# Kernel optimization log

Measured on AMD Instinct MI355X. Metric: run time of the kernel, lower is better.

## Reference

```python
import jax, jax.numpy as jnp
import numpy as np

EPS = 0.01  # eigenvalue cutoff in vstars_from_quadrics


def _cluster(predicted_points, samples, normals):
    # predicted_points: [B,M,3]; samples, normals: [B,N,3]
    B, N, _ = samples.shape
    M = predicted_points.shape[1]

    # --- knn_points with k=1: argmin_m ||s_n - p_m||^2 = argmin_m (|p_m|^2 - 2 s.p) ---
    dots = jnp.einsum('bnd,bmd->bnm', samples, predicted_points)      # [B,N,M]
    pp2 = jnp.sum(predicted_points * predicted_points, axis=-1)       # [B,M]
    closest_idx = jnp.argmin(pp2[:, None, :] - 2.0 * dots, axis=-1)   # [B,N] int

    # --- per-sample plane quadric (ps ps^T), ps = [n, -n.s] ---
    ds = -jnp.sum(normals * samples, axis=-1)                          # [B,N]
    ps = jnp.concatenate([normals, ds[..., None]], axis=-1)            # [B,N,4]
    quadrics = (ps[..., :, None] * ps[..., None, :]).reshape(B, N, 16)  # [B,N,16]

    # --- scatter_mean into M voronoi bins (zero default for empty bins) ---
    seg_sum = jax.vmap(lambda v, i: jax.ops.segment_sum(v, i, num_segments=M))
    q_sum = seg_sum(quadrics, closest_idx)                              # [B,M,16]
    n_sum = seg_sum(normals, closest_idx)                               # [B,M,3]
    cnt = seg_sum(jnp.ones((B, N, 1), quadrics.dtype), closest_idx)     # [B,M,1]
    denom = jnp.maximum(cnt, 1.0)
    target_quadrics = (q_sum / denom).reshape(B, M, 4, 4)
    mean_normals = n_sum / denom

    non_void = jnp.sum(mean_normals * mean_normals, axis=-1) > 0        # [B,M] bool

    # --- vstars_from_quadrics (computed densely, masked where bin is empty) ---
    A = target_quadrics[..., :3, :3]                                    # [B,M,3,3]
    bvec = -target_quadrics[..., 3, :3]                                 # [B,M,3]
    # void bins -> A == 0; substitute a well-conditioned matrix so SVD is safe,
    # result is masked to 0 anyway (rhs is 0 there as well).
    fake = jnp.diag(jnp.asarray([3.0, 2.0, 1.0], A.dtype))
    A_safe = jnp.where(non_void[..., None, None], A, fake)
    u, eigs, vh = jnp.linalg.svd(A_safe)                                # eigs desc
    ratio = eigs / jnp.maximum(eigs[..., 0:1], 1e-20)
    mask_s = ratio > EPS
    eigs2 = jnp.where(mask_s, 1.0 / jnp.where(mask_s, eigs, 1.0), 0.0)  # [B,M,3]
    rhs = bvec - jnp.einsum('bmij,bmj->bmi', A, predicted_points)       # b - A p
    t = jnp.einsum('bmji,bmj->bmi', u, rhs)                             # U^T rhs
    delta = jnp.einsum('bmji,bmj->bmi', vh, eigs2 * t)                  # Vh^T D U^T rhs
    vstars = predicted_points + delta
    vstars = jnp.where(non_void[..., None], vstars, 0.0)
    return A, mean_normals, vstars, non_void


def setup_inputs() -> dict:
    key = jax.random.key(0)
    k1, k2, k3 = jax.random.split(key, 3)
    B, M, N = 4, 1024, 65536
    predicted_points = jax.random.normal(k1, (B, M, 3), dtype=jnp.float32)
    samples = jax.random.normal(k2, (B, N, 3), dtype=jnp.float32)
    normals = jax.random.normal(k3, (B, N, 3), dtype=jnp.float32)
    normals = normals / jnp.linalg.norm(normals, axis=-1, keepdims=True)
    return {"predicted_points": predicted_points, "samples": samples, "normals": normals}


def reference(predicted_points, samples, normals):
    target_As, mean_normals, vstars, non_void = _cluster(predicted_points, samples, normals)
    return target_As, mean_normals, vstars, non_void
```

## Files before the change

kernel.cpp:

```cpp
#include <hip/hip_runtime.h>
#include <hip/hip_cooperative_groups.h>

namespace cg = cooperative_groups;

#define BB 4
#define MM 1024
#define NN 65536
#define CL (BB * MM)

#define ROTJ(APP, AQQ, APQ, ARP, ARQ, V0P, V1P, V2P, V0Q, V1Q, V2Q)            \
    do {                                                                       \
        double apq_ = APQ;                                                     \
        if (fabs(apq_) > 1e-300) {                                             \
            double theta_ = (AQQ - APP) / (2.0 * apq_);                        \
            double t_ = 1.0 / (fabs(theta_) + sqrt(theta_ * theta_ + 1.0));    \
            if (theta_ < 0.0) t_ = -t_;                                        \
            double c_ = 1.0 / sqrt(t_ * t_ + 1.0), sn_ = t_ * c_;              \
            APP -= t_ * apq_; AQQ += t_ * apq_; APQ = 0.0;                     \
            double arp_ = ARP, arq_ = ARQ;                                     \
            ARP = c_ * arp_ - sn_ * arq_;                                      \
            ARQ = sn_ * arp_ + c_ * arq_;                                      \
            double x_;                                                         \
            x_ = V0P; V0P = c_ * x_ - sn_ * V0Q; V0Q = sn_ * x_ + c_ * V0Q;    \
            x_ = V1P; V1P = c_ * x_ - sn_ * V1Q; V1Q = sn_ * x_ + c_ * V1Q;    \
            x_ = V2P; V2P = c_ * x_ - sn_ * V2Q; V2Q = sn_ * x_ + c_ * V2Q;    \
        }                                                                      \
    } while (0)

#define CESWAP(EI, EJ, VA, VB, VC, WA, WB, WC)                                 \
    do {                                                                       \
        if (EI < EJ) {                                                         \
            double tt_;                                                        \
            tt_ = EI; EI = EJ; EJ = tt_;                                       \
            tt_ = VA; VA = WA; WA = tt_;                                       \
            tt_ = VB; VB = WB; WB = tt_;                                       \
            tt_ = VC; VC = WC; WC = tt_;                                       \
        }                                                                      \
    } while (0)

__device__ __forceinline__ void cluster_body(
    int wave, int lane, const float* __restrict__ pp,
    const float* __restrict__ smp, const float* __restrict__ nrm,
    const int* __restrict__ head, const int* __restrict__ next,
    float* __restrict__ out)
{
    const int bc = wave >> 10;
    const int* NX = next + (size_t)bc * NN;
    const float* Sc = smp + (size_t)bc * NN * 3;
    const float* Nr = nrm + (size_t)bc * NN * 3;

    double q00 = 0, q01 = 0, q02 = 0, q11 = 0, q12 = 0, q22 = 0;
    double nd0 = 0, nd1 = 0, nd2 = 0, s0 = 0, s1 = 0, s2 = 0;
    int count = 0;

    int cur = head[wave * 64 + lane];
    while (cur >= 0) {
        double sxv = Sc[cur * 3 + 0], syv = Sc[cur * 3 + 1], szv = Sc[cur * 3 + 2];
        double nx = Nr[cur * 3 + 0], ny = Nr[cur * 3 + 1], nz = Nr[cur * 3 + 2];
        double d = -(nx * sxv + ny * syv + nz * szv);
        q00 += nx * nx; q01 += nx * ny; q02 += nx * nz;
        q11 += ny * ny; q12 += ny * nz; q22 += nz * nz;
        nd0 += nx * d; nd1 += ny * d; nd2 += nz * d;
        s0 += nx; s1 += ny; s2 += nz;
        ++count;
        cur = NX[cur];
    }
#pragma unroll
    for (int o = 32; o > 0; o >>= 1) {
        q00 += __shfl_xor(q00, o); q01 += __shfl_xor(q01, o); q02 += __shfl_xor(q02, o);
        q11 += __shfl_xor(q11, o); q12 += __shfl_xor(q12, o); q22 += __shfl_xor(q22, o);
        nd0 += __shfl_xor(nd0, o); nd1 += __shfl_xor(nd1, o); nd2 += __shfl_xor(nd2, o);
        s0  += __shfl_xor(s0, o);  s1  += __shfl_xor(s1, o);  s2  += __shfl_xor(s2, o);
        count += __shfl_xor(count, o);
    }

    double denom = count > 1 ? (double)count : 1.0;
    double A00 = q00 / denom, A01 = q01 / denom, A02 = q02 / denom;
    double A11 = q11 / denom, A12 = q12 / denom, A22 = q22 / denom;
    double mn0 = s0 / denom, mn1 = s1 / denom, mn2 = s2 / denom;
    double bv0 = -nd0 / denom, bv1 = -nd1 / denom, bv2 = -nd2 / denom;
    bool nonvoid = (mn0 * mn0 + mn1 * mn1 + mn2 * mn2) > 0.0;

    double vs0 = 0, vs1 = 0, vs2 = 0;
    if (nonvoid) {
        double a00 = A00, a01 = A01, a02 = A02, a11 = A11, a12 = A12, a22 = A22;
        double v00 = 1, v01 = 0, v02 = 0;
        double v10 = 0, v11 = 1, v12 = 0;
        double v20 = 0, v21 = 0, v22 = 1;
#pragma unroll
        for (int sweep = 0; sweep < 8; ++sweep) {
            ROTJ(a00, a11, a01, a02, a12, v00, v10, v20, v01, v11, v21);
            ROTJ(a00, a22, a02, a01, a12, v00, v10, v20, v02, v12, v22);
            ROTJ(a11, a22, a12, a01, a02, v01, v11, v21, v02, v12, v22);
        }
        double e0 = a00, e1 = a11, e2 = a22;
        CESWAP(e0, e1, v00, v10, v20, v01, v11, v21);
        CESWAP(e0, e2, v00, v10, v20, v02, v12, v22);
        CESWAP(e1, e2, v01, v11, v21, v02, v12, v22);

        double emax = e0 > 1e-20 ? e0 : 1e-20;
        const float* Pp = pp + (size_t)wave * 3;
        double px = Pp[0], py = Pp[1], pz = Pp[2];
        double r0 = bv0 - (A00 * px + A01 * py + A02 * pz);
        double r1 = bv1 - (A01 * px + A11 * py + A12 * pz);
        double r2 = bv2 - (A02 * px + A12 * py + A22 * pz);
        double thr = 0.01 * emax;
        if (e0 > thr) { double w = (v00 * r0 + v10 * r1 + v20 * r2) / e0; vs0 += w * v00; vs1 += w * v10; vs2 += w * v20; }
        if (e1 > thr) { double w = (v01 * r0 + v11 * r1 + v21 * r2) / e1; vs0 += w * v01; vs1 += w * v11; vs2 += w * v21; }
        if (e2 > thr) { double w = (v02 * r0 + v12 * r1 + v22 * r2) / e2; vs0 += w * v02; vs1 += w * v12; vs2 += w * v22; }
        vs0 += px; vs1 += py; vs2 += pz;
    }

    if (lane == 0) {
        float* Ao = out + (size_t)wave * 9;
        Ao[0] = (float)A00; Ao[1] = (float)A01; Ao[2] = (float)A02;
        Ao[3] = (float)A01; Ao[4] = (float)A11; Ao[5] = (float)A12;
        Ao[6] = (float)A02; Ao[7] = (float)A12; Ao[8] = (float)A22;
        float* Mo = out + 36864 + (size_t)wave * 3;
        Mo[0] = (float)mn0; Mo[1] = (float)mn1; Mo[2] = (float)mn2;
        float* Vo = out + 49152 + (size_t)wave * 3;
        Vo[0] = (float)vs0; Vo[1] = (float)vs1; Vo[2] = (float)vs2;
        out[61440 + wave] = nonvoid ? 1.0f : 0.0f;
    }
}

__global__ __launch_bounds__(512, 4) void k_fused(
    const float* __restrict__ pp, const float* __restrict__ smp,
    const float* __restrict__ nrm, int* __restrict__ head,
    int* __restrict__ next, float* __restrict__ out)
{
    cg::grid_group grid = cg::this_grid();

    __shared__ float4 pts[MM];
    __shared__ float bestSh[8][256];
    __shared__ int   biSh[8][256];

    head[blockIdx.x * 512 + threadIdx.x] = -1;
    const int b   = blockIdx.x >> 7;
    const int blk = blockIdx.x & 127;
    const float* P = pp + b * MM * 3;
    for (int i = threadIdx.x; i < MM; i += 512) {
        float x = P[i * 3 + 0], y = P[i * 3 + 1], z = P[i * 3 + 2];
        pts[i] = make_float4(x, y, z, x * x + y * y + z * z);
    }
    grid.sync();

    const int l = threadIdx.x & 63;
    const int g = threadIdx.x >> 6;
    const float* S = smp + (size_t)b * NN * 3;

    for (int half = 0; half < 2; ++half) {
        const int nb = blk * 512 + half * 256;
        float ax[4], ay[4], az[4], best[4];
        int bi[4];
#pragma unroll
        for (int j = 0; j < 4; ++j) {
            int n = nb + j * 64 + l;
            ax[j] = -2.0f * S[n * 3 + 0];
            ay[j] = -2.0f * S[n * 3 + 1];
            az[j] = -2.0f * S[n * 3 + 2];
            best[j] = 3.4e38f;
            bi[j] = 0;
        }
        const int m0 = g * 128;
#pragma unroll 4
        for (int mi = 0; mi < 128; ++mi) {
            float4 p = pts[m0 + mi];
#pragma unroll
            for (int j = 0; j < 4; ++j) {
                float sc = fmaf(ax[j], p.x, fmaf(ay[j], p.y, fmaf(az[j], p.z, p.w)));
                if (sc < best[j]) { best[j] = sc; bi[j] = m0 + mi; }
            }
        }
#pragma unroll
        for (int j = 0; j < 4; ++j) {
            bestSh[g][j * 64 + l] = best[j];
            biSh[g][j * 64 + l]   = bi[j];
        }
        __syncthreads();

        if (threadIdx.x < 256) {
            const int t = threadIdx.x;
            float bb = bestSh[0][t];
            int   ii = biSh[0][t];
#pragma unroll
            for (int gg = 1; gg < 8; ++gg) {
                float bo = bestSh[gg][t];
                int   io = biSh[gg][t];
                if (bo < bb) { bb = bo; ii = io; }
            }
            const int n = nb + t;
            const int gc = b * MM + ii;
            next[(size_t)b * NN + n] = atomicExch(&head[gc * 64 + (t & 63)], n);
        }
        __syncthreads();
    }
    __threadfence();
    grid.sync();

    cluster_body(blockIdx.x * 8 + g, l, pp, smp, nrm, head, next, out);
}

__global__ __launch_bounds__(256) void k_clear(int4* __restrict__ head4)
{
    head4[blockIdx.x * 256 + threadIdx.x] = make_int4(-1, -1, -1, -1);
}

__global__ __launch_bounds__(512) void k_assign(
    const float* __restrict__ pp, const float* __restrict__ smp,
    int* __restrict__ head, int* __restrict__ next)
{
    __shared__ float4 pts[MM];
    __shared__ float bestSh[8][256];
    __shared__ int   biSh[8][256];

    const int b   = blockIdx.x >> 8;
    const int blk = blockIdx.x & 255;
    const float* P = pp + b * MM * 3;
    for (int i = threadIdx.x; i < MM; i += 512) {
        float x = P[i * 3 + 0], y = P[i * 3 + 1], z = P[i * 3 + 2];
        pts[i] = make_float4(x, y, z, x * x + y * y + z * z);
    }
    __syncthreads();

    const int l  = threadIdx.x & 63;
    const int g  = threadIdx.x >> 6;
    const int nb = blk * 256;
    const float* S = smp + (size_t)b * NN * 3;

    float ax[4], ay[4], az[4], best[4];
    int bi[4];
#pragma unroll
    for (int j = 0; j < 4; ++j) {
        int n = nb + j * 64 + l;
        ax[j] = -2.0f * S[n * 3 + 0];
        ay[j] = -2.0f * S[n * 3 + 1];
        az[j] = -2.0f * S[n * 3 + 2];
        best[j] = 3.4e38f;
        bi[j] = 0;
    }
    const int m0 = g * 128;
#pragma unroll 4
    for (int mi = 0; mi < 128; ++mi) {
        float4 p = pts[m0 + mi];
#pragma unroll
        for (int j = 0; j < 4; ++j) {
            float sc = fmaf(ax[j], p.x, fmaf(ay[j], p.y, fmaf(az[j], p.z, p.w)));
            if (sc < best[j]) { best[j] = sc; bi[j] = m0 + mi; }
        }
    }
#pragma unroll
    for (int j = 0; j < 4; ++j) {
        bestSh[g][j * 64 + l] = best[j];
        biSh[g][j * 64 + l]   = bi[j];
    }
    __syncthreads();

    if (threadIdx.x < 256) {
        const int t = threadIdx.x;
        float bb = bestSh[0][t];
        int   ii = biSh[0][t];
#pragma unroll
        for (int gg = 1; gg < 8; ++gg) {
            float bo = bestSh[gg][t];
            int   io = biSh[gg][t];
            if (bo < bb) { bb = bo; ii = io; }
        }
        const int n = nb + t;
        const int gc = b * MM + ii;
        next[(size_t)b * NN + n] = atomicExch(&head[gc * 64 + (t & 63)], n);
    }
}

__global__ __launch_bounds__(256) void k_cluster(
    const float* __restrict__ pp, const float* __restrict__ smp,
    const float* __restrict__ nrm, const int* __restrict__ head,
    const int* __restrict__ next, float* __restrict__ out)
{
    cluster_body(blockIdx.x * 4 + (threadIdx.x >> 6), threadIdx.x & 63,
                 pp, smp, nrm, head, next, out);
}

extern "C" void kernel_launch(void* const* d_in, const int* in_sizes, int n_in,
                              void* d_out, int out_size, void* d_ws, size_t ws_size,
                              hipStream_t stream)
{
    const float* pp  = (const float*)d_in[0];
    const float* smp = (const float*)d_in[1];
    const float* nrm = (const float*)d_in[2];
    float* out = (float*)d_out;

    int* head = (int*)d_ws;
    int* next = head + CL * 64;

    int maxB = 0;
    hipError_t qe = hipOccupancyMaxActiveBlocksPerMultiprocessor(&maxB, k_fused, 512, 0);
    if (qe == hipSuccess && maxB >= 2) {
        void* args[] = { (void*)&pp, (void*)&smp, (void*)&nrm,
                         (void*)&head, (void*)&next, (void*)&out };
        hipError_t le = hipLaunchCooperativeKernel((const void*)k_fused,
                                                   dim3(512), dim3(512),
                                                   args, 0, stream);
        if (le == hipSuccess) return;
    }
    k_clear<<<256, 256, 0, stream>>>((int4*)head);
    k_assign<<<1024, 512, 0, stream>>>(pp, smp, head, next);
    k_cluster<<<CL / 4, 256, 0, stream>>>(pp, smp, nrm, head, next, out);
}
```

Measured before the change: 71.80 us.

## Replace linked-list bins with fixed-capacity bucket payloads for cluster accumulation

The assignment kernel now takes a slot in the sample's nearest-center bucket with an atomicAdd on a per-cluster counter. It writes a packed float4 (normal, plane offset) into a fixed-capacity bucket, instead of linking the sample into per-lane linked lists. The cluster kernel then reads each bucket contiguously with all 64 lanes, replacing dependent pointer-chasing loads. The cooperative single-launch fused kernel is removed in favour of three ordinary launches. This requires a roughly 64 MB workspace (the old chain path is kept as a fallback) and silently drops samples beyond 1024 per cluster while still counting them in the mean.

```diff
diff --git a/kernel.cpp b/kernel.cpp
--- a/kernel.cpp
+++ b/kernel.cpp
@@ -1,12 +1,10 @@
 #include <hip/hip_runtime.h>
-#include <hip/hip_cooperative_groups.h>
-
-namespace cg = cooperative_groups;
 
 #define BB 4
 #define MM 1024
 #define NN 65536
 #define CL (BB * MM)
+#define CAP 1024
 
 #define ROTJ(APP, AQQ, APQ, ARP, ARQ, V0P, V1P, V2P, V0Q, V1Q, V2Q)            \
     do {                                                                       \
@@ -38,12 +36,250 @@
         }                                                                      \
     } while (0)
 
-__device__ __forceinline__ void cluster_body(
-    int wave, int lane, const float* __restrict__ pp,
-    const float* __restrict__ smp, const float* __restrict__ nrm,
-    const int* __restrict__ head, const int* __restrict__ next,
-    float* __restrict__ out)
-{
+__device__ __forceinline__ void finish_cluster(
+    int wave, int lane, int count,
+    double q00, double q01, double q02, double q11, double q12, double q22,
+    double nd0, double nd1, double nd2, double s0, double s1, double s2,
+    const float* __restrict__ pp, float* __restrict__ out)
+{
+    double denom = count > 1 ? (double)count : 1.0;
+    double A00 = q00 / denom, A01 = q01 / denom, A02 = q02 / denom;
+    double A11 = q11 / denom, A12 = q12 / denom, A22 = q22 / denom;
+    double mn0 = s0 / denom, mn1 = s1 / denom, mn2 = s2 / denom;
+    double bv0 = -nd0 / denom, bv1 = -nd1 / denom, bv2 = -nd2 / denom;
+    bool nonvoid = (mn0 * mn0 + mn1 * mn1 + mn2 * mn2) > 0.0;
+
+    double vs0 = 0, vs1 = 0, vs2 = 0;
+    if (nonvoid) {
+        double a00 = A00, a01 = A01, a02 = A02, a11 = A11, a12 = A12, a22 = A22;
+        double v00 = 1, v01 = 0, v02 = 0;
+        double v10 = 0, v11 = 1, v12 = 0;
+        double v20 = 0, v21 = 0, v22 = 1;
+#pragma unroll
+        for (int sweep = 0; sweep < 8; ++sweep) {
+            ROTJ(a00, a11, a01, a02, a12, v00, v10, v20, v01, v11, v21);
+            ROTJ(a00, a22, a02, a01, a12, v00, v10, v20, v02, v12, v22);
+            ROTJ(a11, a22, a12, a01, a02, v01, v11, v21, v02, v12, v22);
+        }
+        double e0 = a00, e1 = a11, e2 = a22;
+        CESWAP(e0, e1, v00, v10, v20, v01, v11, v21);
+        CESWAP(e0, e2, v00, v10, v20, v02, v12, v22);
+        CESWAP(e1, e2, v01, v11, v21, v02, v12, v22);
+
+        double emax = e0 > 1e-20 ? e0 : 1e-20;
+        const float* Pp = pp + (size_t)wave * 3;
+        double px = Pp[0], py = Pp[1], pz = Pp[2];
+        double r0 = bv0 - (A00 * px + A01 * py + A02 * pz);
+        double r1 = bv1 - (A01 * px + A11 * py + A12 * pz);
+        double r2 = bv2 - (A02 * px + A12 * py + A22 * pz);
+        double thr = 0.01 * emax;
+        if (e0 > thr) { double w = (v00 * r0 + v10 * r1 + v20 * r2) / e0; vs0 += w * v00; vs1 += w * v10; vs2 += w * v20; }
+        if (e1 > thr) { double w = (v01 * r0 + v11 * r1 + v21 * r2) / e1; vs0 += w * v01; vs1 += w * v11; vs2 += w * v21; }
+        if (e2 > thr) { double w = (v02 * r0 + v12 * r1 + v22 * r2) / e2; vs0 += w * v02; vs1 += w * v12; vs2 += w * v22; }
+        vs0 += px; vs1 += py; vs2 += pz;
+    }
+
+    if (lane == 0) {
+        float* Ao = out + (size_t)wave * 9;
+        Ao[0] = (float)A00; Ao[1] = (float)A01; Ao[2] = (float)A02;
+        Ao[3] = (float)A01; Ao[4] = (float)A11; Ao[5] = (float)A12;
+        Ao[6] = (float)A02; Ao[7] = (float)A12; Ao[8] = (float)A22;
+        float* Mo = out + 36864 + (size_t)wave * 3;
+        Mo[0] = (float)mn0; Mo[1] = (float)mn1; Mo[2] = (float)mn2;
+        float* Vo = out + 49152 + (size_t)wave * 3;
+        Vo[0] = (float)vs0; Vo[1] = (float)vs1; Vo[2] = (float)vs2;
+        out[61440 + wave] = nonvoid ? 1.0f : 0.0f;
+    }
+}
+
+__global__ __launch_bounds__(256) void k_clear_cnt(int4* __restrict__ cnt4)
+{
+    cnt4[blockIdx.x * 256 + threadIdx.x] = make_int4(0, 0, 0, 0);
+}
+
+__global__ __launch_bounds__(512) void k_assign_bucket(
+    const float* __restrict__ pp, const float* __restrict__ smp,
+    const float* __restrict__ nrm, int* __restrict__ cnt,
+    float4* __restrict__ payload)
+{
+    __shared__ float4 pts[MM];
+    __shared__ float bestSh[8][256];
+    __shared__ int   biSh[8][256];
+
+    const int b   = blockIdx.x >> 8;
+    const int blk = blockIdx.x & 255;
+    const float* P = pp + b * MM * 3;
+    for (int i = threadIdx.x; i < MM; i += 512) {
+        float x = P[i * 3 + 0], y = P[i * 3 + 1], z = P[i * 3 + 2];
+        pts[i] = make_float4(x, y, z, x * x + y * y + z * z);
+    }
+    __syncthreads();
+
+    const int l  = threadIdx.x & 63;
+    const int g  = threadIdx.x >> 6;
+    const int nb = blk * 256;
+    const float* S = smp + (size_t)b * NN * 3;
+
+    float ax[4], ay[4], az[4], best[4];
+    int bi[4];
+#pragma unroll
+    for (int j = 0; j < 4; ++j) {
+        int n = nb + j * 64 + l;
+        ax[j] = -2.0f * S[n * 3 + 0];
+        ay[j] = -2.0f * S[n * 3 + 1];
+        az[j] = -2.0f * S[n * 3 + 2];
+        best[j] = 3.4e38f;
+        bi[j] = 0;
+    }
+    const int m0 = g * 128;
+#pragma unroll 4
+    for (int mi = 0; mi < 128; ++mi) {
+        float4 p = pts[m0 + mi];
+#pragma unroll
+        for (int j = 0; j < 4; ++j) {
+            float sc = fmaf(ax[j], p.x, fmaf(ay[j], p.y, fmaf(az[j], p.z, p.w)));
+            if (sc < best[j]) { best[j] = sc; bi[j] = m0 + mi; }
+        }
+    }
+#pragma unroll
+    for (int j = 0; j < 4; ++j) {
+        bestSh[g][j * 64 + l] = best[j];
+        biSh[g][j * 64 + l]   = bi[j];
+    }
+    __syncthreads();
+
+    if (threadIdx.x < 256) {
+        const int t = threadIdx.x;
+        float bb = bestSh[0][t];
+        int   ii = biSh[0][t];
+#pragma unroll
+        for (int gg = 1; gg < 8; ++gg) {
+            float bo = bestSh[gg][t];
+            int   io = biSh[gg][t];
+            if (bo < bb) { bb = bo; ii = io; }
+        }
+        const int n = nb + t;
+        const int gc = b * MM + ii;
+
+        const float* Nr = nrm + (size_t)b * NN * 3;
+        float sx = S[n * 3 + 0], sy = S[n * 3 + 1], sz = S[n * 3 + 2];
+        float nx = Nr[n * 3 + 0], ny = Nr[n * 3 + 1], nz = Nr[n * 3 + 2];
+        float d = -(nx * sx + ny * sy + nz * sz);
+
+        int pos = atomicAdd(&cnt[gc], 1);
+        if (pos < CAP) payload[((size_t)gc << 10) + pos] = make_float4(nx, ny, nz, d);
+    }
+}
+
+__global__ __launch_bounds__(256) void k_cluster_bucket(
+    const float* __restrict__ pp, const float4* __restrict__ payload,
+    const int* __restrict__ cnt, float* __restrict__ out)
+{
+    const int wave = blockIdx.x * 4 + (threadIdx.x >> 6);
+    const int lane = threadIdx.x & 63;
+    const int count = cnt[wave];
+    const int stored = count < CAP ? count : CAP;
+    const float4* PL = payload + ((size_t)wave << 10);
+
+    double q00 = 0, q01 = 0, q02 = 0, q11 = 0, q12 = 0, q22 = 0;
+    double nd0 = 0, nd1 = 0, nd2 = 0, s0 = 0, s1 = 0, s2 = 0;
+    for (int i = lane; i < stored; i += 64) {
+        float4 pl = PL[i];
+        double nx = pl.x, ny = pl.y, nz = pl.z, d = pl.w;
+        q00 += nx * nx; q01 += nx * ny; q02 += nx * nz;
+        q11 += ny * ny; q12 += ny * nz; q22 += nz * nz;
+        nd0 += nx * d; nd1 += ny * d; nd2 += nz * d;
+        s0 += nx; s1 += ny; s2 += nz;
+    }
+#pragma unroll
+    for (int o = 32; o > 0; o >>= 1) {
+        q00 += __shfl_xor(q00, o); q01 += __shfl_xor(q01, o); q02 += __shfl_xor(q02, o);
+        q11 += __shfl_xor(q11, o); q12 += __shfl_xor(q12, o); q22 += __shfl_xor(q22, o);
+        nd0 += __shfl_xor(nd0, o); nd1 += __shfl_xor(nd1, o); nd2 += __shfl_xor(nd2, o);
+        s0  += __shfl_xor(s0, o);  s1  += __shfl_xor(s1, o);  s2  += __shfl_xor(s2, o);
+    }
+    finish_cluster(wave, lane, count, q00, q01, q02, q11, q12, q22,
+                   nd0, nd1, nd2, s0, s1, s2, pp, out);
+}
+
+__global__ __launch_bounds__(256) void k_clear(int4* __restrict__ head4)
+{
+    head4[blockIdx.x * 256 + threadIdx.x] = make_int4(-1, -1, -1, -1);
+}
+
+__global__ __launch_bounds__(512) void k_assign_chain(
+    const float* __restrict__ pp, const float* __restrict__ smp,
+    int* __restrict__ head, int* __restrict__ next)
+{
+    __shared__ float4 pts[MM];
+    __shared__ float bestSh[8][256];
+    __shared__ int   biSh[8][256];
+
+    const int b   = blockIdx.x >> 8;
+    const int blk = blockIdx.x & 255;
+    const float* P = pp + b * MM * 3;
+    for (int i = threadIdx.x; i < MM; i += 512) {
+        float x = P[i * 3 + 0], y = P[i * 3 + 1], z = P[i * 3 + 2];
+        pts[i] = make_float4(x, y, z, x * x + y * y + z * z);
+    }
+    __syncthreads();
+
+    const int l  = threadIdx.x & 63;
+    const int g  = threadIdx.x >> 6;
+    const int nb = blk * 256;
+    const float* S = smp + (size_t)b * NN * 3;
+
+    float ax[4], ay[4], az[4], best[4];
+    int bi[4];
+#pragma unroll
+    for (int j = 0; j < 4; ++j) {
+        int n = nb + j * 64 + l;
+        ax[j] = -2.0f * S[n * 3 + 0];
+        ay[j] = -2.0f * S[n * 3 + 1];
+        az[j] = -2.0f * S[n * 3 + 2];
+        best[j] = 3.4e38f;
+        bi[j] = 0;
+    }
+    const int m0 = g * 128;
+#pragma unroll 4
+    for (int mi = 0; mi < 128; ++mi) {
+        float4 p = pts[m0 + mi];
+#pragma unroll
+        for (int j = 0; j < 4; ++j) {
+            float sc = fmaf(ax[j], p.x, fmaf(ay[j], p.y, fmaf(az[j], p.z, p.w)));
+            if (sc < best[j]) { best[j] = sc; bi[j] = m0 + mi; }
+        }
+    }
+#pragma unroll
+    for (int j = 0; j < 4; ++j) {
+        bestSh[g][j * 64 + l] = best[j];
+        biSh[g][j * 64 + l]   = bi[j];
+    }
+    __syncthreads();
+
+    if (threadIdx.x < 256) {
+        const int t = threadIdx.x;
+        float bb = bestSh[0][t];
+        int   ii = biSh[0][t];
+#pragma unroll
+        for (int gg = 1; gg < 8; ++gg) {
+            float bo = bestSh[gg][t];
+            int   io = biSh[gg][t];
+            if (bo < bb) { bb = bo; ii = io; }
+        }
+        const int n = nb + t;
+        const int gc = b * MM + ii;
+        next[(size_t)b * NN + n] = atomicExch(&head[gc * 64 + (t & 63)], n);
+    }
+}
+
+__global__ __launch_bounds__(256) void k_cluster_chain(
+    const float* __restrict__ pp, const float* __restrict__ smp,
+    const float* __restrict__ nrm, const int* __restrict__ head,
+    const int* __restrict__ next, float* __restrict__ out)
+{
+    const int wave = blockIdx.x * 4 + (threadIdx.x >> 6);
+    const int lane = threadIdx.x & 63;
     const int bc = wave >> 10;
     const int* NX = next + (size_t)bc * NN;
     const float* Sc = smp + (size_t)bc * NN * 3;
@@ -73,212 +309,8 @@
         s0  += __shfl_xor(s0, o);  s1  += __shfl_xor(s1, o);  s2  += __shfl_xor(s2, o);
         count += __shfl_xor(count, o);
     }
-
-    double denom = count > 1 ? (double)count : 1.0;
-    double A00 = q00 / denom, A01 = q01 / denom, A02 = q02 / denom;
-    double A11 = q11 / denom, A12 = q12 / denom, A22 = q22 / denom;
-    double mn0 = s0 / denom, mn1 = s1 / denom, mn2 = s2 / denom;
-    double bv0 = -nd0 / denom, bv1 = -nd1 / denom, bv2 = -nd2 / denom;
-    bool nonvoid = (mn0 * mn0 + mn1 * mn1 + mn2 * mn2) > 0.0;
-
-    double vs0 = 0, vs1 = 0, vs2 = 0;
-    if (nonvoid) {
-        double a00 = A00, a01 = A01, a02 = A02, a11 = A11, a12 = A12, a22 = A22;
-        double v00 = 1, v01 = 0, v02 = 0;
-        double v10 = 0, v11 = 1, v12 = 0;
-        double v20 = 0, v21 = 0, v22 = 1;
-#pragma unroll
-        for (int sweep = 0; sweep < 8; ++sweep) {
-            ROTJ(a00, a11, a01, a02, a12, v00, v10, v20, v01, v11, v21);
-            ROTJ(a00, a22, a02, a01, a12, v00, v10, v20, v02, v12, v22);
-            ROTJ(a11, a22, a12, a01, a02, v01, v11, v21, v02, v12, v22);
-        }
-        double e0 = a00, e1 = a11, e2 = a22;
-        CESWAP(e0, e1, v00, v10, v20, v01, v11, v21);
-        CESWAP(e0, e2, v00, v10, v20, v02, v12, v22);
-        CESWAP(e1, e2, v01, v11, v21, v02, v12, v22);
-
-        double emax = e0 > 1e-20 ? e0 : 1e-20;
-        const float* Pp = pp + (size_t)wave * 3;
-        double px = Pp[0], py = Pp[1], pz = Pp[2];
-        double r0 = bv0 - (A00 * px + A01 * py + A02 * pz);
-        double r1 = bv1 - (A01 * px + A11 * py + A12 * pz);
-        double r2 = bv2 - (A02 * px + A12 * py + A22 * pz);
-        double thr = 0.01 * emax;
-        if (e0 > thr) { double w = (v00 * r0 + v10 * r1 + v20 * r2) / e0; vs0 += w * v00; vs1 += w * v10; vs2 += w * v20; }
-        if (e1 > thr) { double w = (v01 * r0 + v11 * r1 + v21 * r2) / e1; vs0 += w * v01; vs1 += w * v11; vs2 += w * v21; }
-        if (e2 > thr) { double w = (v02 * r0 + v12 * r1 + v22 * r2) / e2; vs0 += w * v02; vs1 += w * v12; vs2 += w * v22; }
-        vs0 += px; vs1 += py; vs2 += pz;
-    }
-
-    if (lane == 0) {
-        float* Ao = out + (size_t)wave * 9;
-        Ao[0] = (float)A00; Ao[1] = (float)A01; Ao[2] = (float)A02;
-        Ao[3] = (float)A01; Ao[4] = (float)A11; Ao[5] = (float)A12;
-        Ao[6] = (float)A02; Ao[7] = (float)A12; Ao[8] = (float)A22;
-        float* Mo = out + 36864 + (size_t)wave * 3;
-        Mo[0] = (float)mn0; Mo[1] = (float)mn1; Mo[2] = (float)mn2;
-        float* Vo = out + 49152 + (size_t)wave * 3;
-        Vo[0] = (float)vs0; Vo[1] = (float)vs1; Vo[2] = (float)vs2;
-        out[61440 + wave] = nonvoid ? 1.0f : 0.0f;
-    }
-}
-
-__global__ __launch_bounds__(512, 4) void k_fused(
-    const float* __restrict__ pp, const float* __restrict__ smp,
-    const float* __restrict__ nrm, int* __restrict__ head,
-    int* __restrict__ next, float* __restrict__ out)
-{
-    cg::grid_group grid = cg::this_grid();
-
-    __shared__ float4 pts[MM];
-    __shared__ float bestSh[8][256];
-    __shared__ int   biSh[8][256];
-
-    head[blockIdx.x * 512 + threadIdx.x] = -1;
-    const int b   = blockIdx.x >> 7;
-    const int blk = blockIdx.x & 127;
-    const float* P = pp + b * MM * 3;
-    for (int i = threadIdx.x; i < MM; i += 512) {
-        float x = P[i * 3 + 0], y = P[i * 3 + 1], z = P[i * 3 + 2];
-        pts[i] = make_float4(x, y, z, x * x + y * y + z * z);
-    }
-    grid.sync();
-
-    const int l = threadIdx.x & 63;
-    const int g = threadIdx.x >> 6;
-    const float* S = smp + (size_t)b * NN * 3;
-
-    for (int half = 0; half < 2; ++half) {
-        const int nb = blk * 512 + half * 256;
-        float ax[4], ay[4], az[4], best[4];
-        int bi[4];
-#pragma unroll
-        for (int j = 0; j < 4; ++j) {
-            int n = nb + j * 64 + l;
-            ax[j] = -2.0f * S[n * 3 + 0];
-            ay[j] = -2.0f * S[n * 3 + 1];
-            az[j] = -2.0f * S[n * 3 + 2];
-            best[j] = 3.4e38f;
-            bi[j] = 0;
-        }
-        const int m0 = g * 128;
-#pragma unroll 4
-        for (int mi = 0; mi < 128; ++mi) {
-            float4 p = pts[m0 + mi];
-#pragma unroll
-            for (int j = 0; j < 4; ++j) {
-                float sc = fmaf(ax[j], p.x, fmaf(ay[j], p.y, fmaf(az[j], p.z, p.w)));
-                if (sc < best[j]) { best[j] = sc; bi[j] = m0 + mi; }
-            }
-        }
-#pragma unroll
-        for (int j = 0; j < 4; ++j) {
-            bestSh[g][j * 64 + l] = best[j];
-            biSh[g][j * 64 + l]   = bi[j];
-        }
-        __syncthreads();
-
-        if (threadIdx.x < 256) {
-            const int t = threadIdx.x;
-            float bb = bestSh[0][t];
-            int   ii = biSh[0][t];
-#pragma unroll
-            for (int gg = 1; gg < 8; ++gg) {
-                float bo = bestSh[gg][t];
-                int   io = biSh[gg][t];
-                if (bo < bb) { bb = bo; ii = io; }
-            }
-            const int n = nb + t;
-            const int gc = b * MM + ii;
-            next[(size_t)b * NN + n] = atomicExch(&head[gc * 64 + (t & 63)], n);
-        }
-        __syncthreads();
-    }
-    __threadfence();
-    grid.sync();
-
-    cluster_body(blockIdx.x * 8 + g, l, pp, smp, nrm, head, next, out);
-}
-
-__global__ __launch_bounds__(256) void k_clear(int4* __restrict__ head4)
-{
-    head4[blockIdx.x * 256 + threadIdx.x] = make_int4(-1, -1, -1, -1);
-}
-
-__global__ __launch_bounds__(512) void k_assign(
-    const float* __restrict__ pp, const float* __restrict__ smp,
-    int* __restrict__ head, int* __restrict__ next)
-{
-    __shared__ float4 pts[MM];
-    __shared__ float bestSh[8][256];
-    __shared__ int   biSh[8][256];
-
-    const int b   = blockIdx.x >> 8;
-    const int blk = blockIdx.x & 255;
-    const float* P = pp + b * MM * 3;
-    for (int i = threadIdx.x; i < MM; i += 512) {
-        float x = P[i * 3 + 0], y = P[i * 3 + 1], z = P[i * 3 + 2];
-        pts[i] = make_float4(x, y, z, x * x + y * y + z * z);
-    }
-    __syncthreads();
-
-    const int l  = threadIdx.x & 63;
-    const int g  = threadIdx.x >> 6;
-    const int nb = blk * 256;
-    const float* S = smp + (size_t)b * NN * 3;
-
-    float ax[4], ay[4], az[4], best[4];
-    int bi[4];
-#pragma unroll
-    for (int j = 0; j < 4; ++j) {
-        int n = nb + j * 64 + l;
-        ax[j] = -2.0f * S[n * 3 + 0];
-        ay[j] = -2.0f * S[n * 3 + 1];
-        az[j] = -2.0f * S[n * 3 + 2];
-        best[j] = 3.4e38f;
-        bi[j] = 0;
-    }
-    const int m0 = g * 128;
-#pragma unroll 4
-    for (int mi = 0; mi < 128; ++mi) {
-        float4 p = pts[m0 + mi];
-#pragma unroll
-        for (int j = 0; j < 4; ++j) {
-            float sc = fmaf(ax[j], p.x, fmaf(ay[j], p.y, fmaf(az[j], p.z, p.w)));
-            if (sc < best[j]) { best[j] = sc; bi[j] = m0 + mi; }
-        }
-    }
-#pragma unroll
-    for (int j = 0; j < 4; ++j) {
-        bestSh[g][j * 64 + l] = best[j];
-        biSh[g][j * 64 + l]   = bi[j];
-    }
-    __syncthreads();
-
-    if (threadIdx.x < 256) {
-        const int t = threadIdx.x;
-        float bb = bestSh[0][t];
-        int   ii = biSh[0][t];
-#pragma unroll
-        for (int gg = 1; gg < 8; ++gg) {
-            float bo = bestSh[gg][t];
-            int   io = biSh[gg][t];
-            if (bo < bb) { bb = bo; ii = io; }
-        }
-        const int n = nb + t;
-        const int gc = b * MM + ii;
-        next[(size_t)b * NN + n] = atomicExch(&head[gc * 64 + (t & 63)], n);
-    }
-}
-
-__global__ __launch_bounds__(256) void k_cluster(
-    const float* __restrict__ pp, const float* __restrict__ smp,
-    const float* __restrict__ nrm, const int* __restrict__ head,
-    const int* __restrict__ next, float* __restrict__ out)
-{
-    cluster_body(blockIdx.x * 4 + (threadIdx.x >> 6), threadIdx.x & 63,
-                 pp, smp, nrm, head, next, out);
+    finish_cluster(wave, lane, count, q00, q01, q02, q11, q12, q22,
+                   nd0, nd1, nd2, s0, s1, s2, pp, out);
 }
 
 extern "C" void kernel_launch(void* const* d_in, const int* in_sizes, int n_in,
@@ -290,20 +322,18 @@
     const float* nrm = (const float*)d_in[2];
     float* out = (float*)d_out;
 
-    int* head = (int*)d_ws;
-    int* next = head + CL * 64;
-
-    int maxB = 0;
-    hipError_t qe = hipOccupancyMaxActiveBlocksPerMultiprocessor(&maxB, k_fused, 512, 0);
-    if (qe == hipSuccess && maxB >= 2) {
-        void* args[] = { (void*)&pp, (void*)&smp, (void*)&nrm,
-                         (void*)&head, (void*)&next, (void*)&out };
-        hipError_t le = hipLaunchCooperativeKernel((const void*)k_fused,
-                                                   dim3(512), dim3(512),
-                                                   args, 0, stream);
-        if (le == hipSuccess) return;
-    }
-    k_clear<<<256, 256, 0, stream>>>((int4*)head);
-    k_assign<<<1024, 512, 0, stream>>>(pp, smp, head, next);
-    k_cluster<<<CL / 4, 256, 0, stream>>>(pp, smp, nrm, head, next, out);
-}
+    const size_t bucket_need = 65536 + (size_t)CL * CAP * 16;
+    if (ws_size >= bucket_need) {
+        int*    cnt     = (int*)d_ws;
+        float4* payload = (float4*)((char*)d_ws + 65536);
+        k_clear_cnt<<<4, 256, 0, stream>>>((int4*)cnt);
+        k_assign_bucket<<<1024, 512, 0, stream>>>(pp, smp, nrm, cnt, payload);
+        k_cluster_bucket<<<CL / 4, 256, 0, stream>>>(pp, payload, cnt, out);
+    } else {
+        int* head = (int*)d_ws;
+        int* next = head + CL * 64;
+        k_clear<<<256, 256, 0, stream>>>((int4*)head);
+        k_assign_chain<<<1024, 512, 0, stream>>>(pp, smp, head, next);
+        k_cluster_chain<<<CL / 4, 256, 0, stream>>>(pp, smp, nrm, head, next, out);
+    }
+}
```

Measured after the change: 86.18 us. +20.0%, slower.
